# Optimization experiments

Hardware: AMD Instinct MI355X
Metric: run time of the kernel (lower is better)

Reference implementation:

```python
import jax, jax.numpy as jnp
import numpy as np

D_MODEL = 1024
D_STATE = 16
BATCH = 2
SEQ = 2048


def setup_inputs() -> dict:
    key = jax.random.key(0)
    k1, k2, k3, k4 = jax.random.split(key, 4)
    x = jax.random.normal(k1, (BATCH, SEQ, D_MODEL), dtype=jnp.float32)
    dt = jax.random.uniform(k2, (BATCH, SEQ, D_MODEL), dtype=jnp.float32)
    B_in = jax.random.normal(k3, (BATCH, SEQ, D_STATE), dtype=jnp.float32)
    C_in = jax.random.normal(k4, (BATCH, SEQ, D_STATE), dtype=jnp.float32)
    # Parameters, initialized as in the torch module
    A = jnp.arange(1, D_STATE + 1, dtype=jnp.float32)[None, :] * jnp.ones((D_MODEL, 1), jnp.float32)
    A_log = jnp.log(A)
    D = jnp.ones((D_MODEL,), jnp.float32)
    return {"x": x, "dt": dt, "B_in": B_in, "C_in": C_in, "A_log": A_log, "D": D}


def reference(x, dt, B_in, C_in, A_log, D):
    # x, dt: (b, L, d);  B_in, C_in: (b, L, n);  A_log: (d, n);  D: (d,)
    A = -jnp.exp(A_log)                                   # (d, n)
    A_disc = jnp.exp(dt[..., None] * A[None, None])       # (b, L, d, n)
    Bx = dt[..., None] * B_in[:, :, None, :] * x[..., None]  # (b, L, d, n)

    def step(state, inputs):
        a_t, bx_t, c_t = inputs                            # (b,d,n),(b,d,n),(b,n)
        state = a_t * state + bx_t                         # (b, d, n)
        y_t = jnp.einsum('bdn,bn->bd', state, c_t)         # (b, d)
        return state, y_t

    state0 = jnp.zeros((x.shape[0], x.shape[2], A_log.shape[1]), x.dtype)
    # scan over the time axis (put L first)
    _, y = jax.lax.scan(
        step, state0,
        (jnp.moveaxis(A_disc, 1, 0), jnp.moveaxis(Bx, 1, 0), jnp.moveaxis(C_in, 1, 0)))
    y = jnp.moveaxis(y, 0, 1)                              # (b, L, d)
    return y + x * D[None, None, :]
```

## Files before the change

kernel.cpp:

```cpp
#include <hip/hip_runtime.h>
#include <hip/hip_bf16.h>

namespace {

constexpr int kB = 2;
constexpr int kL = 2048;
constexpr int kD = 1024;
constexpr int kN = 16;
constexpr int kTPB = 256;
constexpr int kNDBLK = kD / kTPB;
constexpr int kBD = kB * kD;
constexpr int kBDN = kBD * kN;
constexpr float kLog2e = 1.4426950408889634f;

__device__ __forceinline__ float ex2(float v) {
  return __builtin_amdgcn_exp2f(v);
}

__device__ __forceinline__ void build_pows(float e1, float* a) {
  const float p2 = e1 * e1;
  const float p4 = p2 * p2;
  const float p8 = p4 * p4;
  a[0] = e1;      a[1] = p2;      a[2] = p2 * e1; a[3] = p4;
  a[4] = p4 * e1; a[5] = p4 * p2; a[6] = p4 * a[2]; a[7] = p8;
  a[8] = p8 * e1; a[9] = p8 * p2; a[10] = p8 * a[2]; a[11] = p8 * p4;
  a[12] = p8 * a[4]; a[13] = p8 * a[5]; a[14] = p8 * a[6]; a[15] = p8 * p8;
}

template <int C>
__global__ __launch_bounds__(kTPB) void ssm_phase1(
    const float* __restrict__ x, const float* __restrict__ dt,
    const float* __restrict__ Bin, const float* __restrict__ Alog,
    float* __restrict__ WS, float* __restrict__ SDT) {
  constexpr int LC = kL / C;
  const int bid = blockIdx.x;
  const int c = bid % C;
  const int r = bid / C;
  const int dblk = r % kNDBLK;
  const int b = r / kNDBLK;
  const int d = dblk * kTPB + threadIdx.x;

  float AnL[kN];
  const float* al = Alog + d * kN;
#pragma unroll
  for (int n = 0; n < kN; ++n) AnL[n] = -__expf(al[n]) * kLog2e;
  bool fast = true;
#pragma unroll
  for (int n = 1; n < kN; ++n)
    fast = fast && (fabsf(AnL[n] - (float)(n + 1) * AnL[0]) <=
                    1e-4f * fabsf(AnL[n]));

  float s[kN];
#pragma unroll
  for (int n = 0; n < kN; ++n) s[n] = 0.f;
  float sdt = 0.f;

  const int t0 = c * LC;
  const float* xp = x + ((size_t)b * kL + t0) * kD + d;
  const float* dp = dt + ((size_t)b * kL + t0) * kD + d;
  const float* bp = Bin + ((size_t)b * kL + t0) * kN;

  if (fast) {
    const float A0 = AnL[0];
#pragma unroll 4
    for (int tt = 0; tt < LC; ++tt) {
      const float dtv = dp[(size_t)tt * kD];
      const float xv = xp[(size_t)tt * kD];
      sdt += dtv;
      const float dtx = dtv * xv;
      float a[kN];
      build_pows(ex2(dtv * A0), a);
#pragma unroll
      for (int n = 0; n < kN; ++n)
        s[n] = fmaf(a[n], s[n], dtx * bp[tt * kN + n]);
    }
  } else {
#pragma unroll 2
    for (int tt = 0; tt < LC; ++tt) {
      const float dtv = dp[(size_t)tt * kD];
      const float xv = xp[(size_t)tt * kD];
      sdt += dtv;
      const float dtx = dtv * xv;
#pragma unroll
      for (int n = 0; n < kN; ++n) {
        const float a = ex2(dtv * AnL[n]);
        s[n] = fmaf(a, s[n], dtx * bp[tt * kN + n]);
      }
    }
  }

  const size_t bd = (size_t)b * kD + d;
#pragma unroll
  for (int n = 0; n < kN; ++n)
    WS[(size_t)c * kBDN + (size_t)n * kBD + bd] = s[n];
  SDT[(size_t)c * kBD + bd] = sdt;
}

template <int C>
__global__ __launch_bounds__(256) void ssm_phase2(
    const float* __restrict__ WS, const float* __restrict__ SDT,
    const float* __restrict__ Alog, float* __restrict__ WI) {
  const int i = blockIdx.x * 256 + threadIdx.x;
  const int n = i >> 11;
  const int bd = i & (kBD - 1);
  const int d = bd & (kD - 1);
  const float An = -__expf(Alog[d * kN + n]) * kLog2e;
  float carry = 0.f;
  for (int c = 0; c < C; ++c) {
    const size_t idx = (size_t)c * kBDN + i;
    const float a = ex2(An * SDT[(size_t)c * kBD + bd]);
    WI[idx] = carry;
    carry = fmaf(a, carry, WS[idx]);
  }
}

template <int C>
__global__ __launch_bounds__(kTPB) void ssm_phase3(
    const float* __restrict__ x, const float* __restrict__ dt,
    const float* __restrict__ Bin, const float* __restrict__ Cin,
    const float* __restrict__ Alog, const float* __restrict__ Dp,
    const float* __restrict__ WI, float* __restrict__ y) {
  constexpr int LC = kL / C;
  const int bid = blockIdx.x;
  const int c = bid % C;
  const int r = bid / C;
  const int dblk = r % kNDBLK;
  const int b = r / kNDBLK;
  const int d = dblk * kTPB + threadIdx.x;

  float AnL[kN];
  const float* al = Alog + d * kN;
#pragma unroll
  for (int n = 0; n < kN; ++n) AnL[n] = -__expf(al[n]) * kLog2e;
  bool fast = true;
#pragma unroll
  for (int n = 1; n < kN; ++n)
    fast = fast && (fabsf(AnL[n] - (float)(n + 1) * AnL[0]) <=
                    1e-4f * fabsf(AnL[n]));

  float s[kN];
  const size_t bd = (size_t)b * kD + d;
#pragma unroll
  for (int n = 0; n < kN; ++n)
    s[n] = WI[(size_t)c * kBDN + (size_t)n * kBD + bd];

  const float Dv = Dp[d];

  const int t0 = c * LC;
  const float* xp = x + ((size_t)b * kL + t0) * kD + d;
  const float* dp = dt + ((size_t)b * kL + t0) * kD + d;
  const float* bp = Bin + ((size_t)b * kL + t0) * kN;
  const float* cp = Cin + ((size_t)b * kL + t0) * kN;
  float* yp = y + ((size_t)b * kL + t0) * kD + d;

  if (fast) {
    const float A0 = AnL[0];
#pragma unroll 4
    for (int tt = 0; tt < LC; ++tt) {
      const float dtv = dp[(size_t)tt * kD];
      const float xv = xp[(size_t)tt * kD];
      const float dtx = dtv * xv;
      float a[kN];
      build_pows(ex2(dtv * A0), a);
      float acc = 0.f;
#pragma unroll
      for (int n = 0; n < kN; ++n) {
        s[n] = fmaf(a[n], s[n], dtx * bp[tt * kN + n]);
        acc = fmaf(s[n], cp[tt * kN + n], acc);
      }
      yp[(size_t)tt * kD] = fmaf(xv, Dv, acc);
    }
  } else {
#pragma unroll 2
    for (int tt = 0; tt < LC; ++tt) {
      const float dtv = dp[(size_t)tt * kD];
      const float xv = xp[(size_t)tt * kD];
      const float dtx = dtv * xv;
      float acc = 0.f;
#pragma unroll
      for (int n = 0; n < kN; ++n) {
        const float a = ex2(dtv * AnL[n]);
        s[n] = fmaf(a, s[n], dtx * bp[tt * kN + n]);
        acc = fmaf(s[n], cp[tt * kN + n], acc);
      }
      yp[(size_t)tt * kD] = fmaf(xv, Dv, acc);
    }
  }
}

__global__ __launch_bounds__(256) void ssm_seq(
    const float* __restrict__ x, const float* __restrict__ dt,
    const float* __restrict__ Bin, const float* __restrict__ Cin,
    const float* __restrict__ Alog, const float* __restrict__ Dp,
    float* __restrict__ y) {
  const int gid = blockIdx.x * 256 + threadIdx.x;
  if (gid >= kB * kD) return;
  const int b = gid / kD;
  const int d = gid % kD;

  float AnL[kN];
  const float* al = Alog + d * kN;
#pragma unroll
  for (int n = 0; n < kN; ++n) AnL[n] = -__expf(al[n]) * kLog2e;

  float s[kN];
#pragma unroll
  for (int n = 0; n < kN; ++n) s[n] = 0.f;
  const float Dv = Dp[d];

  const float* xp = x + (size_t)b * kL * kD + d;
  const float* dp = dt + (size_t)b * kL * kD + d;
  const float* bp = Bin + (size_t)b * kL * kN;
  const float* cp = Cin + (size_t)b * kL * kN;
  float* yp = y + (size_t)b * kL * kD + d;

  for (int t = 0; t < kL; ++t) {
    const float dtv = dp[(size_t)t * kD];
    const float xv = xp[(size_t)t * kD];
    const float dtx = dtv * xv;
    float acc = 0.f;
#pragma unroll
    for (int n = 0; n < kN; ++n) {
      const float a = ex2(dtv * AnL[n]);
      s[n] = fmaf(a, s[n], dtx * bp[t * kN + n]);
      acc = fmaf(s[n], cp[t * kN + n], acc);
    }
    yp[(size_t)t * kD] = fmaf(xv, Dv, acc);
  }
}

template <int C>
void launch_chunked(const float* x, const float* dtp, const float* Bin,
                    const float* Cin, const float* Alog, const float* Dp,
                    float* y, float* ws, hipStream_t stream) {
  float* WS = ws;
  float* SDT = WS + (size_t)C * kBDN;
  float* WI = SDT + (size_t)C * kBD;
  const int g = C * kB * kNDBLK;
  ssm_phase1<C><<<g, kTPB, 0, stream>>>(x, dtp, Bin, Alog, WS, SDT);
  ssm_phase2<C><<<kBDN / 256, 256, 0, stream>>>(WS, SDT, Alog, WI);
  ssm_phase3<C><<<g, kTPB, 0, stream>>>(x, dtp, Bin, Cin, Alog, Dp, WI, y);
}

}

extern "C" void kernel_launch(void* const* d_in, const int* in_sizes, int n_in,
                              void* d_out, int out_size, void* d_ws, size_t ws_size,
                              hipStream_t stream) {
  const float* x    = (const float*)d_in[0];
  const float* dtp  = (const float*)d_in[1];
  const float* Bin  = (const float*)d_in[2];
  const float* Cin  = (const float*)d_in[3];
  const float* Alog = (const float*)d_in[4];
  const float* Dp   = (const float*)d_in[5];
  float* y = (float*)d_out;
  float* ws = (float*)d_ws;

  auto need = [](int C) {
    return (size_t)(2 * C * kBDN + C * kBD) * sizeof(float);
  };

  if (ws_size >= need(128)) {
    launch_chunked<128>(x, dtp, Bin, Cin, Alog, Dp, y, ws, stream);
  } else if (ws_size >= need(64)) {
    launch_chunked<64>(x, dtp, Bin, Cin, Alog, Dp, y, ws, stream);
  } else if (ws_size >= need(16)) {
    launch_chunked<16>(x, dtp, Bin, Cin, Alog, Dp, y, ws, stream);
  } else {
    ssm_seq<<<(kB * kD + 255) / 256, 256, 0, stream>>>(x, dtp, Bin, Cin, Alog,
                                                       Dp, y);
  }
}
```

Baseline: 41.55 us.

## Stage B/C chunks in LDS and switch chunk-state workspace to n-contiguous layout

Phase 1 and phase 3 now copy each chunk's B (and C) rows into shared memory before the scan, instead of reading them from global memory on every step. The chunk-state workspace changes from n-major to n-innermost so each thread can read and write its 16 states with float4 accesses. Phase 2 is remapped so that consecutive threads cover consecutive n and uses smaller blocks. The shared-memory staging adds a barrier and LDS traffic per block. The new workspace layout makes phase 2 accesses strided by 16 across the bd dimension.

Measured after the change: 47.07 us. 1.13x slower.

```diff
diff --git a/kernel.cpp b/kernel.cpp
--- a/kernel.cpp
+++ b/kernel.cpp
@@ -21,11 +21,12 @@
   const float p2 = e1 * e1;
   const float p4 = p2 * p2;
   const float p8 = p4 * p4;
-  a[0] = e1;      a[1] = p2;      a[2] = p2 * e1; a[3] = p4;
+  a[0] = e1;      a[1] = p2;      a[2] = p2 * e1;  a[3] = p4;
   a[4] = p4 * e1; a[5] = p4 * p2; a[6] = p4 * a[2]; a[7] = p8;
   a[8] = p8 * e1; a[9] = p8 * p2; a[10] = p8 * a[2]; a[11] = p8 * p4;
   a[12] = p8 * a[4]; a[13] = p8 * a[5]; a[14] = p8 * a[6]; a[15] = p8 * p8;
 }
+
 
 template <int C>
 __global__ __launch_bounds__(kTPB) void ssm_phase1(
@@ -38,27 +39,41 @@
   const int r = bid / C;
   const int dblk = r % kNDBLK;
   const int b = r / kNDBLK;
-  const int d = dblk * kTPB + threadIdx.x;
+  const int tid = threadIdx.x;
+  const int d = dblk * kTPB + tid;
+  const int t0 = c * LC;
+
+  __shared__ float Bs[LC * kN];
+  for (int j = tid; j < LC * kN; j += kTPB)
+    Bs[j] = Bin[((size_t)b * kL + t0) * kN + j];
 
   float AnL[kN];
-  const float* al = Alog + d * kN;
-#pragma unroll
-  for (int n = 0; n < kN; ++n) AnL[n] = -__expf(al[n]) * kLog2e;
+  {
+    const float4* alv = reinterpret_cast<const float4*>(Alog + (size_t)d * kN);
+#pragma unroll
+    for (int q = 0; q < 4; ++q) {
+      const float4 v = alv[q];
+      AnL[4 * q + 0] = -__expf(v.x) * kLog2e;
+      AnL[4 * q + 1] = -__expf(v.y) * kLog2e;
+      AnL[4 * q + 2] = -__expf(v.z) * kLog2e;
+      AnL[4 * q + 3] = -__expf(v.w) * kLog2e;
+    }
+  }
   bool fast = true;
 #pragma unroll
   for (int n = 1; n < kN; ++n)
     fast = fast && (fabsf(AnL[n] - (float)(n + 1) * AnL[0]) <=
                     1e-4f * fabsf(AnL[n]));
 
+  __syncthreads();
+
   float s[kN];
 #pragma unroll
   for (int n = 0; n < kN; ++n) s[n] = 0.f;
   float sdt = 0.f;
 
-  const int t0 = c * LC;
   const float* xp = x + ((size_t)b * kL + t0) * kD + d;
   const float* dp = dt + ((size_t)b * kL + t0) * kD + d;
-  const float* bp = Bin + ((size_t)b * kL + t0) * kN;
 
   if (fast) {
     const float A0 = AnL[0];
@@ -72,7 +87,7 @@
       build_pows(ex2(dtv * A0), a);
 #pragma unroll
       for (int n = 0; n < kN; ++n)
-        s[n] = fmaf(a[n], s[n], dtx * bp[tt * kN + n]);
+        s[n] = fmaf(a[n], s[n], dtx * Bs[tt * kN + n]);
     }
   } else {
 #pragma unroll 2
@@ -82,32 +97,32 @@
       sdt += dtv;
       const float dtx = dtv * xv;
 #pragma unroll
-      for (int n = 0; n < kN; ++n) {
-        const float a = ex2(dtv * AnL[n]);
-        s[n] = fmaf(a, s[n], dtx * bp[tt * kN + n]);
-      }
+      for (int n = 0; n < kN; ++n)
+        s[n] = fmaf(ex2(dtv * AnL[n]), s[n], dtx * Bs[tt * kN + n]);
     }
   }
 
   const size_t bd = (size_t)b * kD + d;
-#pragma unroll
-  for (int n = 0; n < kN; ++n)
-    WS[(size_t)c * kBDN + (size_t)n * kBD + bd] = s[n];
+  float4* wsv = reinterpret_cast<float4*>(WS + ((size_t)c * kBD + bd) * kN);
+#pragma unroll
+  for (int q = 0; q < 4; ++q)
+    wsv[q] = make_float4(s[4 * q], s[4 * q + 1], s[4 * q + 2], s[4 * q + 3]);
   SDT[(size_t)c * kBD + bd] = sdt;
 }
 
 template <int C>
-__global__ __launch_bounds__(256) void ssm_phase2(
+__global__ __launch_bounds__(128) void ssm_phase2(
     const float* __restrict__ WS, const float* __restrict__ SDT,
     const float* __restrict__ Alog, float* __restrict__ WI) {
-  const int i = blockIdx.x * 256 + threadIdx.x;
-  const int n = i >> 11;
-  const int bd = i & (kBD - 1);
+  const int i = blockIdx.x * 128 + threadIdx.x;
+  const int bd = i >> 4;
+  const int n = i & 15;
   const int d = bd & (kD - 1);
-  const float An = -__expf(Alog[d * kN + n]) * kLog2e;
+  const float An = -__expf(Alog[(size_t)d * kN + n]) * kLog2e;
   float carry = 0.f;
+#pragma unroll 8
   for (int c = 0; c < C; ++c) {
-    const size_t idx = (size_t)c * kBDN + i;
+    const size_t idx = ((size_t)c * kBD + bd) * kN + n;
     const float a = ex2(An * SDT[(size_t)c * kBD + bd]);
     WI[idx] = carry;
     carry = fmaf(a, carry, WS[idx]);
@@ -126,31 +141,55 @@
   const int r = bid / C;
   const int dblk = r % kNDBLK;
   const int b = r / kNDBLK;
-  const int d = dblk * kTPB + threadIdx.x;
+  const int tid = threadIdx.x;
+  const int d = dblk * kTPB + tid;
+  const int t0 = c * LC;
+
+  __shared__ float Bs[LC * kN];
+  __shared__ float Cs[LC * kN];
+  for (int j = tid; j < LC * kN; j += kTPB) {
+    Bs[j] = Bin[((size_t)b * kL + t0) * kN + j];
+    Cs[j] = Cin[((size_t)b * kL + t0) * kN + j];
+  }
 
   float AnL[kN];
-  const float* al = Alog + d * kN;
-#pragma unroll
-  for (int n = 0; n < kN; ++n) AnL[n] = -__expf(al[n]) * kLog2e;
+  {
+    const float4* alv = reinterpret_cast<const float4*>(Alog + (size_t)d * kN);
+#pragma unroll
+    for (int q = 0; q < 4; ++q) {
+      const float4 v = alv[q];
+      AnL[4 * q + 0] = -__expf(v.x) * kLog2e;
+      AnL[4 * q + 1] = -__expf(v.y) * kLog2e;
+      AnL[4 * q + 2] = -__expf(v.z) * kLog2e;
+      AnL[4 * q + 3] = -__expf(v.w) * kLog2e;
+    }
+  }
   bool fast = true;
 #pragma unroll
   for (int n = 1; n < kN; ++n)
     fast = fast && (fabsf(AnL[n] - (float)(n + 1) * AnL[0]) <=
                     1e-4f * fabsf(AnL[n]));
 
+  __syncthreads();
+
   float s[kN];
   const size_t bd = (size_t)b * kD + d;
-#pragma unroll
-  for (int n = 0; n < kN; ++n)
-    s[n] = WI[(size_t)c * kBDN + (size_t)n * kBD + bd];
+  {
+    const float4* wiv =
+        reinterpret_cast<const float4*>(WI + ((size_t)c * kBD + bd) * kN);
+#pragma unroll
+    for (int q = 0; q < 4; ++q) {
+      const float4 v = wiv[q];
+      s[4 * q + 0] = v.x;
+      s[4 * q + 1] = v.y;
+      s[4 * q + 2] = v.z;
+      s[4 * q + 3] = v.w;
+    }
+  }
 
   const float Dv = Dp[d];
-
-  const int t0 = c * LC;
   const float* xp = x + ((size_t)b * kL + t0) * kD + d;
   const float* dp = dt + ((size_t)b * kL + t0) * kD + d;
-  const float* bp = Bin + ((size_t)b * kL + t0) * kN;
-  const float* cp = Cin + ((size_t)b * kL + t0) * kN;
   float* yp = y + ((size_t)b * kL + t0) * kD + d;
 
   if (fast) {
@@ -165,8 +204,8 @@
       float acc = 0.f;
 #pragma unroll
       for (int n = 0; n < kN; ++n) {
-        s[n] = fmaf(a[n], s[n], dtx * bp[tt * kN + n]);
-        acc = fmaf(s[n], cp[tt * kN + n], acc);
+        s[n] = fmaf(a[n], s[n], dtx * Bs[tt * kN + n]);
+        acc = fmaf(s[n], Cs[tt * kN + n], acc);
       }
       yp[(size_t)tt * kD] = fmaf(xv, Dv, acc);
     }
@@ -179,9 +218,8 @@
       float acc = 0.f;
 #pragma unroll
       for (int n = 0; n < kN; ++n) {
-        const float a = ex2(dtv * AnL[n]);
-        s[n] = fmaf(a, s[n], dtx * bp[tt * kN + n]);
-        acc = fmaf(s[n], cp[tt * kN + n], acc);
+        s[n] = fmaf(ex2(dtv * AnL[n]), s[n], dtx * Bs[tt * kN + n]);
+        acc = fmaf(s[n], Cs[tt * kN + n], acc);
       }
       yp[(size_t)tt * kD] = fmaf(xv, Dv, acc);
     }
@@ -199,7 +237,7 @@
   const int d = gid % kD;
 
   float AnL[kN];
-  const float* al = Alog + d * kN;
+  const float* al = Alog + (size_t)d * kN;
 #pragma unroll
   for (int n = 0; n < kN; ++n) AnL[n] = -__expf(al[n]) * kLog2e;
 
@@ -238,7 +276,7 @@
   float* WI = SDT + (size_t)C * kBD;
   const int g = C * kB * kNDBLK;
   ssm_phase1<C><<<g, kTPB, 0, stream>>>(x, dtp, Bin, Alog, WS, SDT);
-  ssm_phase2<C><<<kBDN / 256, 256, 0, stream>>>(WS, SDT, Alog, WI);
+  ssm_phase2<C><<<kBDN / 128, 128, 0, stream>>>(WS, SDT, Alog, WI);
   ssm_phase3<C><<<g, kTPB, 0, stream>>>(x, dtp, Bin, Cin, Alog, Dp, WI, y);
 }
 
```
